# Kernel tuning notes

Measured on AMD Instinct MI355X. Metric: run time of the kernel, lower is better.

The kernel has to match this reference:

```python
import jax, jax.numpy as jnp
import numpy as np

N_NODES = 50000
N_EDGES = 800000
IN_DIM = 128
NUM_GRAPHS = 64
NEG_SLOPE = 0.2  # PyG GATConv default


def _gat_layer(x, src, dst, W, a_s, a_d, b):
    """PyG GATConv (concat=True), eval mode (no dropout).
    x: [N, Fin]; W: [H*C, Fin]; a_s, a_d: [H, C]; b: [H*C]."""
    N = x.shape[0]
    H, C = a_s.shape
    h = (x @ W.T).reshape(N, H, C)                      # [N,H,C]
    es = jnp.einsum('nhc,hc->nh', h, a_s)               # [N,H]
    ed = jnp.einsum('nhc,hc->nh', h, a_d)               # [N,H]
    e = jax.nn.leaky_relu(es[src] + ed[dst], NEG_SLOPE)  # [E,H]
    # segment softmax over incoming edges of each destination node
    m = jax.ops.segment_max(e, dst, num_segments=N)     # [N,H]
    ex = jnp.exp(e - m[dst])
    denom = jax.ops.segment_sum(ex, dst, num_segments=N)
    alpha = ex / denom[dst]                             # [E,H]
    out = jax.ops.segment_sum(h[src] * alpha[:, :, None], dst, num_segments=N)
    return out.reshape(N, H * C) + b


def _make_params(key):
    dims = [(512, IN_DIM, 8, 64), (256, 512, 8, 32), (128, 256, 8, 16), (512, 128, 8, 64)]
    ps = {}
    k = key
    for i, (out_f, in_f, H, C) in enumerate(dims, 1):
        k, k1, k2, k3 = jax.random.split(k, 4)
        s = 1.0 / np.sqrt(in_f)
        ps[f'W{i}'] = jax.random.normal(k1, (out_f, in_f), jnp.float32) * s
        ps[f'a{i}s'] = jax.random.normal(k2, (H, C), jnp.float32) * 0.1
        ps[f'a{i}d'] = jax.random.normal(k3, (H, C), jnp.float32) * 0.1
        ps[f'b{i}'] = jnp.zeros((out_f,), jnp.float32)
    k, k1, k2 = jax.random.split(k, 3)
    ps['lw1'] = jax.random.normal(k1, (32, 512), jnp.float32) * (1.0 / np.sqrt(512))
    ps['lb1'] = jnp.zeros((32,), jnp.float32)
    ps['lw2'] = jax.random.normal(k2, (2, 32), jnp.float32) * (1.0 / np.sqrt(32))
    ps['lb2'] = jnp.zeros((2,), jnp.float32)
    return ps


def setup_inputs() -> dict:
    key = jax.random.key(0)
    kx, ke, kb, kp = jax.random.split(key, 4)
    x = jax.random.normal(kx, (N_NODES, IN_DIM), jnp.float32)
    edge_index = jax.random.randint(ke, (2, N_EDGES), 0, N_NODES, jnp.int64 if jax.config.jax_enable_x64 else jnp.int32)
    batch = jnp.sort(jax.random.randint(kb, (N_NODES,), 0, NUM_GRAPHS, edge_index.dtype))
    inp = {'x': x, 'edge_index': edge_index, 'batch': batch}
    inp.update(_make_params(kp))
    return inp


def reference(x, edge_index, batch,
              W1, a1s, a1d, b1, W2, a2s, a2d, b2,
              W3, a3s, a3d, b3, W4, a4s, a4d, b4,
              lw1, lb1, lw2, lb2):
    N = x.shape[0]
    # PyG GATConv add_self_loops=True
    loop = jnp.arange(N, dtype=edge_index.dtype)
    src = jnp.concatenate([edge_index[0], loop])
    dst = jnp.concatenate([edge_index[1], loop])

    h = jax.nn.elu(_gat_layer(x, src, dst, W1, a1s, a1d, b1))
    h = jax.nn.elu(_gat_layer(h, src, dst, W2, a2s, a2d, b2))
    h = jax.nn.elu(_gat_layer(h, src, dst, W3, a3s, a3d, b3))
    h = _gat_layer(h, src, dst, W4, a4s, a4d, b4)

    # global mean pool over graphs
    sums = jax.ops.segment_sum(h, batch, num_segments=NUM_GRAPHS)
    cnts = jax.ops.segment_sum(jnp.ones((N, 1), h.dtype), batch, num_segments=NUM_GRAPHS)
    g = sums / jnp.maximum(cnts, 1.0)                   # [G, 512]

    g = jax.nn.elu(g @ lw1.T + lb1)                     # dropout skipped (eval)
    return g @ lw2.T + lb2                              # [G, 2]
```

## Files before the change

### kernel.cpp

```cpp
#include <hip/hip_runtime.h>
#include <math.h>

#define NN 50000
#define NE 800000
#define NEP (NE + NN)
#define NGR 64
#define NHEAD 8
#define MPAD 50048

typedef short short8 __attribute__((ext_vector_type(8)));
typedef float floatx4 __attribute__((ext_vector_type(4)));
typedef unsigned uintx4 __attribute__((ext_vector_type(4)));

__device__ inline float bf2f(short s) {
    union { unsigned u; float f; } v;
    v.u = ((unsigned)(unsigned short)s) << 16;
    return v.f;
}
__device__ inline float bf2f_lo(unsigned p) {
    union { unsigned u; float f; } v; v.u = p << 16; return v.f;
}
__device__ inline float bf2f_hi(unsigned p) {
    union { unsigned u; float f; } v; v.u = p & 0xffff0000u; return v.f;
}
__device__ inline short f2bf(float f) {
    union { float f; unsigned u; } v; v.f = f;
    unsigned r = v.u + 0x7fffu + ((v.u >> 16) & 1u);
    return (short)(r >> 16);
}

__global__ void count_deg(const int* __restrict__ ei, int* __restrict__ deg) {
    int e = blockIdx.x * 256 + threadIdx.x;
    if (e >= NEP) return;
    int d = (e < NE) ? ei[NE + e] : (e - NE);
    atomicAdd(&deg[d], 1);
}

__global__ __launch_bounds__(1024) void scan_local(const int* __restrict__ deg,
                                                   int* __restrict__ out,
                                                   int* __restrict__ bsum, int n) {
    __shared__ int sd[1024];
    int b = blockIdx.x, t = threadIdx.x;
    int i = b * 1024 + t;
    int v = (i < n) ? deg[i] : 0;
    sd[t] = v;
    __syncthreads();
    for (int off = 1; off < 1024; off <<= 1) {
        int tmp = (t >= off) ? sd[t - off] : 0;
        __syncthreads();
        sd[t] += tmp;
        __syncthreads();
    }
    if (i < n) out[i] = sd[t] - v;
    if (t == 1023) bsum[b] = sd[1023];
}

__global__ void scan_bsum(int* __restrict__ bsum, int nb) {
    if (threadIdx.x == 0) {
        int s = 0;
        for (int i = 0; i < nb; i++) { int v = bsum[i]; bsum[i] = s; s += v; }
        bsum[nb] = s;
    }
}

__global__ void scan_add(int* __restrict__ row_ptr, int* __restrict__ cursor,
                         const int* __restrict__ bsum, int n, int nb) {
    int i = blockIdx.x * 256 + threadIdx.x;
    if (i < n) {
        int v = row_ptr[i] + bsum[i >> 10];
        row_ptr[i] = v;
        cursor[i] = v;
    } else if (i == n) {
        row_ptr[n] = bsum[nb];
    }
}

__global__ void scatter_edges(const int* __restrict__ ei, int* __restrict__ cursor,
                              int* __restrict__ srcs) {
    int e = blockIdx.x * 256 + threadIdx.x;
    if (e >= NEP) return;
    int s, d;
    if (e < NE) { s = ei[e]; d = ei[NE + e]; }
    else        { s = e - NE; d = e - NE; }
    int pos = atomicAdd(&cursor[d], 1);
    srcs[pos] = s;
}

__global__ void conv_f2bf(const float* __restrict__ in, short* __restrict__ out, int n) {
    int i = blockIdx.x * 256 + threadIdx.x;
    if (i < n) out[i] = f2bf(in[i]);
}

__global__ void conv_x_pad4(const float* __restrict__ x, short* __restrict__ xb) {
    int i = blockIdx.x * 256 + threadIdx.x;
    if (i >= MPAD * 32) return;
    int r = i >> 5;
    short4 o;
    if (r < NN) {
        float4 v = *(const float4*)&x[(size_t)i * 4];
        o.x = f2bf(v.x); o.y = f2bf(v.y); o.z = f2bf(v.z); o.w = f2bf(v.w);
    } else {
        o.x = o.y = o.z = o.w = 0;
    }
    *(short4*)&xb[(size_t)i * 4] = o;
}

#define LDA 72
template <int C>
__global__ __launch_bounds__(256) void gemm_bf(const short* __restrict__ A,
                                               const short* __restrict__ B,
                                               short* __restrict__ Cout,
                                               const float* __restrict__ a_s,
                                               const float* __restrict__ a_d,
                                               float* __restrict__ es,
                                               float* __restrict__ ed,
                                               int K) {
    constexpr int Nc = 8 * C;
    constexpr int colTiles = Nc / 128;
    constexpr int JPH = C / 16;
    constexpr int HPW = 64 / C;
    __shared__ __align__(16) short As[128 * LDA];
    __shared__ __align__(16) short Bs[128 * LDA];
    int bx = blockIdx.x % colTiles;
    int by = blockIdx.x / colTiles;
    int row0 = by * 128, col0 = bx * 128;
    int t = threadIdx.x;
    int lane = t & 63, w = t >> 6;
    int wr = (w >> 1) * 64, wc = (w & 1) * 64;
    int lrow = lane & 15, lq = lane >> 4;

    floatx4 acc[4][4];
#pragma unroll
    for (int i = 0; i < 4; i++)
#pragma unroll
        for (int j = 0; j < 4; j++) acc[i][j] = (floatx4)0.0f;

    for (int k0 = 0; k0 < K; k0 += 64) {
#pragma unroll
        for (int i = 0; i < 4; i++) {
            int chunk = t + i * 256;
            int r = chunk >> 3;
            int kc = (chunk & 7) * 8;
            *(short8*)&As[r * LDA + kc] = *(const short8*)&A[(size_t)(row0 + r) * K + k0 + kc];
            *(short8*)&Bs[r * LDA + kc] = *(const short8*)&B[(size_t)(col0 + r) * K + k0 + kc];
        }
        __syncthreads();
#pragma unroll
        for (int kk = 0; kk < 2; kk++) {
            short8 af[4], bfr[4];
#pragma unroll
            for (int i = 0; i < 4; i++)
                af[i] = *(const short8*)&As[(wr + i * 16 + lrow) * LDA + kk * 32 + lq * 8];
#pragma unroll
            for (int j = 0; j < 4; j++)
                bfr[j] = *(const short8*)&Bs[(wc + j * 16 + lrow) * LDA + kk * 32 + lq * 8];
#pragma unroll
            for (int i = 0; i < 4; i++)
#pragma unroll
                for (int j = 0; j < 4; j++)
                    acc[i][j] = __builtin_amdgcn_mfma_f32_16x16x32_bf16(af[i], bfr[j], acc[i][j], 0, 0, 0);
        }
        __syncthreads();
    }

#pragma unroll
    for (int i = 0; i < 4; i++)
#pragma unroll
        for (int j = 0; j < 4; j++)
#pragma unroll
            for (int r = 0; r < 4; r++) {
                int row = row0 + wr + i * 16 + lq * 4 + r;
                int col = col0 + wc + j * 16 + lrow;
                Cout[(size_t)row * Nc + col] = f2bf(acc[i][j][r]);
            }

    float asv[4], adv[4];
#pragma unroll
    for (int j = 0; j < 4; j++) {
        int colA = col0 + wc + j * 16 + lrow;
        asv[j] = a_s[colA];
        adv[j] = a_d[colA];
    }
    int hb = (col0 + wc) / C;
#pragma unroll
    for (int i = 0; i < 4; i++)
#pragma unroll
        for (int r = 0; r < 4; r++) {
            float s_h[HPW], d_h[HPW];
#pragma unroll
            for (int hh = 0; hh < HPW; hh++) { s_h[hh] = 0.f; d_h[hh] = 0.f; }
#pragma unroll
            for (int j = 0; j < 4; j++) {
                s_h[j / JPH] = fmaf(acc[i][j][r], asv[j], s_h[j / JPH]);
                d_h[j / JPH] = fmaf(acc[i][j][r], adv[j], d_h[j / JPH]);
            }
#pragma unroll
            for (int hh = 0; hh < HPW; hh++) {
#pragma unroll
                for (int off = 1; off <= 8; off <<= 1) {
                    s_h[hh] += __shfl_xor(s_h[hh], off);
                    d_h[hh] += __shfl_xor(d_h[hh], off);
                }
            }
            if (lrow == 0) {
                int row = row0 + wr + i * 16 + lq * 4 + r;
                if (row < NN) {
#pragma unroll
                    for (int hh = 0; hh < HPW; hh++) {
                        es[row * 8 + hb + hh] = s_h[hh];
                        ed[row * 8 + hb + hh] = d_h[hh];
                    }
                }
            }
        }
}

template <int C, bool ELU>
__global__ __launch_bounds__(256) void attn_wave(const short* __restrict__ h,
                                                 const float* __restrict__ es,
                                                 const float* __restrict__ ed,
                                                 const int* __restrict__ row_ptr,
                                                 const int* __restrict__ srcs,
                                                 const float* __restrict__ bias,
                                                 short* __restrict__ out) {
    constexpr int HC = NHEAD * C;
    constexpr int TPR = HC / 8;
    constexpr int EPI = 64 / TPR;
    int wave = threadIdx.x >> 6, lane = threadIdx.x & 63;
    int n = blockIdx.x * 4 + wave;
    int start = row_ptr[n];
    int deg = row_ptr[n + 1] - start;
    int hh1 = lane & 7;
    float edv = ed[n * 8 + hh1];

    float pm = -1e30f;
    for (int idx = lane; idx < deg * 8; idx += 64) {
        int s = srcs[start + (idx >> 3)];
        float e = es[s * 8 + hh1] + edv;
        e = e > 0.f ? e : 0.2f * e;
        pm = fmaxf(pm, e);
    }
    pm = fmaxf(pm, __shfl_xor(pm, 8));
    pm = fmaxf(pm, __shfl_xor(pm, 16));
    pm = fmaxf(pm, __shfl_xor(pm, 32));

    float ps = 0.f;
    for (int idx = lane; idx < deg * 8; idx += 64) {
        int s = srcs[start + (idx >> 3)];
        float e = es[s * 8 + hh1] + edv;
        e = e > 0.f ? e : 0.2f * e;
        ps += __expf(e - pm);
    }
    ps += __shfl_xor(ps, 8);
    ps += __shfl_xor(ps, 16);
    ps += __shfl_xor(ps, 32);
    float invd = 1.0f / ps;

    int sub = lane & (TPR - 1);
    int c0 = sub * 8;
    int hh = c0 / C;
    float mh3 = __shfl(pm, hh);
    float iv3 = __shfl(invd, hh);
    float ed3 = __shfl(edv, hh);

    float acc[8];
#pragma unroll
    for (int j = 0; j < 8; j++) acc[j] = 0.f;

    for (int k = lane / TPR; k < deg; k += EPI) {
        int s = srcs[start + k];
        float e = es[s * 8 + hh] + ed3;
        e = e > 0.f ? e : 0.2f * e;
        float wv = __expf(e - mh3) * iv3;
        uintx4 hv = *(const uintx4*)&h[(size_t)s * HC + c0];
#pragma unroll
        for (int j = 0; j < 4; j++) {
            acc[2 * j]     = fmaf(wv, bf2f_lo(hv[j]), acc[2 * j]);
            acc[2 * j + 1] = fmaf(wv, bf2f_hi(hv[j]), acc[2 * j + 1]);
        }
    }
    if (EPI >= 2) {
#pragma unroll
        for (int j = 0; j < 8; j++) acc[j] += __shfl_xor(acc[j], 32);
    }
    if (EPI == 4) {
#pragma unroll
        for (int j = 0; j < 8; j++) acc[j] += __shfl_xor(acc[j], 16);
    }
    if (lane < TPR) {
        floatx4 b0 = *(const floatx4*)&bias[c0];
        floatx4 b1 = *(const floatx4*)&bias[c0 + 4];
        float bb[8] = {b0[0], b0[1], b0[2], b0[3], b1[0], b1[1], b1[2], b1[3]};
        unsigned pk[4];
#pragma unroll
        for (int j = 0; j < 4; j++) {
            float o0 = acc[2 * j] + bb[2 * j];
            float o1 = acc[2 * j + 1] + bb[2 * j + 1];
            if (ELU) {
                o0 = o0 > 0.f ? o0 : (__expf(o0) - 1.0f);
                o1 = o1 > 0.f ? o1 : (__expf(o1) - 1.0f);
            }
            pk[j] = ((unsigned)(unsigned short)f2bf(o0)) |
                    (((unsigned)(unsigned short)f2bf(o1)) << 16);
        }
        *(uintx4*)&out[(size_t)n * HC + c0] = *(uintx4*)pk;
    }
}

__global__ __launch_bounds__(256) void pool_kernel(const short* __restrict__ h,
                                                   const int* __restrict__ batch,
                                                   float* __restrict__ gout) {
    __shared__ float red[256];
    int g = blockIdx.x >> 3;
    int fc = (blockIdx.x & 7) * 64;
    int lo = 0, hi = NN;
    while (lo < hi) { int mid = (lo + hi) >> 1; if (batch[mid] < g) lo = mid + 1; else hi = mid; }
    int s = lo;
    lo = 0; hi = NN;
    while (lo < hi) { int mid = (lo + hi) >> 1; if (batch[mid] < g + 1) lo = mid + 1; else hi = mid; }
    int e = lo;
    int t = threadIdx.x;
    int f = t & 63, stripe = t >> 6;
    float a = 0.f;
    for (int r = s + stripe; r < e; r += 4)
        a += bf2f(h[(size_t)r * 512 + fc + f]);
    red[t] = a;
    __syncthreads();
    if (t < 128) red[t] += red[t + 128];
    __syncthreads();
    if (t < 64) {
        float inv = 1.0f / fmaxf((float)(e - s), 1.0f);
        gout[g * 512 + fc + t] = (red[t] + red[t + 64]) * inv;
    }
}

__global__ __launch_bounds__(64) void mlp_kernel(const float* __restrict__ g,
                                                 const float* __restrict__ lw1,
                                                 const float* __restrict__ lb1,
                                                 const float* __restrict__ lw2,
                                                 const float* __restrict__ lb2,
                                                 float* __restrict__ outp) {
    __shared__ float gv[512];
    __shared__ float y1[32];
    int b = blockIdx.x, t = threadIdx.x;
    for (int i = t; i < 512; i += 64) gv[i] = g[b * 512 + i];
    __syncthreads();
    if (t < 32) {
        float a = lb1[t];
        for (int k = 0; k < 512; k++) a = fmaf(gv[k], lw1[t * 512 + k], a);
        y1[t] = a > 0.f ? a : (__expf(a) - 1.0f);
    }
    __syncthreads();
    if (t < 2) {
        float a = lb2[t];
        for (int k = 0; k < 32; k++) a = fmaf(y1[k], lw2[t * 32 + k], a);
        outp[b * 2 + t] = a;
    }
}

extern "C" void kernel_launch(void* const* d_in, const int* in_sizes, int n_in,
                              void* d_out, int out_size, void* d_ws, size_t ws_size,
                              hipStream_t stream) {
    (void)in_sizes; (void)n_in; (void)out_size; (void)ws_size;
    const float* x     = (const float*)d_in[0];
    const int*   ei    = (const int*)d_in[1];
    const int*   batch = (const int*)d_in[2];
    const float* W[4]  = {(const float*)d_in[3], (const float*)d_in[7],
                          (const float*)d_in[11], (const float*)d_in[15]};
    const float* As_[4] = {(const float*)d_in[4], (const float*)d_in[8],
                           (const float*)d_in[12], (const float*)d_in[16]};
    const float* Ad_[4] = {(const float*)d_in[5], (const float*)d_in[9],
                           (const float*)d_in[13], (const float*)d_in[17]};
    const float* Bi[4]  = {(const float*)d_in[6], (const float*)d_in[10],
                           (const float*)d_in[14], (const float*)d_in[18]};
    const float* lw1 = (const float*)d_in[19];
    const float* lb1 = (const float*)d_in[20];
    const float* lw2 = (const float*)d_in[21];
    const float* lb2 = (const float*)d_in[22];
    float* out = (float*)d_out;

    short* Ab = (short*)d_ws;
    short* Hb = Ab + (size_t)MPAD * 512;
    short* Wb = Hb + (size_t)MPAD * 512;
    short* Wb_[4] = {Wb, Wb + 65536, Wb + 196608, Wb + 229376};
    const int wsz[4] = {65536, 131072, 32768, 65536};
    float* esb  = (float*)(Wb + 294912);
    float* edb  = esb + NN * NHEAD;
    float* gbuf = edb + NN * NHEAD;
    int* row_ptr = (int*)(gbuf + NGR * 512);
    int* cursor  = row_ptr + (NN + 1);
    int* srcs    = cursor + (NN + 1);
    int* bsum    = srcs + NEP;

    const int nblk = (NN + 1023) / 1024;

    hipMemsetAsync(cursor, 0, NN * sizeof(int), stream);
    count_deg<<<(NEP + 255) / 256, 256, 0, stream>>>(ei, cursor);
    scan_local<<<nblk, 1024, 0, stream>>>(cursor, row_ptr, bsum, NN);
    scan_bsum<<<1, 64, 0, stream>>>(bsum, nblk);
    scan_add<<<(NN + 256) / 256, 256, 0, stream>>>(row_ptr, cursor, bsum, NN, nblk);
    scatter_edges<<<(NEP + 255) / 256, 256, 0, stream>>>(ei, cursor, srcs);

    conv_x_pad4<<<(MPAD * 32 + 255) / 256, 256, 0, stream>>>(x, Ab);
    for (int i = 0; i < 4; i++)
        conv_f2bf<<<(wsz[i] + 255) / 256, 256, 0, stream>>>(W[i], Wb_[i], wsz[i]);

    const int rowTiles = MPAD / 128;
    const int ag = NN / 4;

    gemm_bf<64><<<rowTiles * 4, 256, 0, stream>>>(Ab, Wb_[0], Hb, As_[0], Ad_[0], esb, edb, 128);
    attn_wave<64, true><<<ag, 256, 0, stream>>>(Hb, esb, edb, row_ptr, srcs, Bi[0], Ab);

    gemm_bf<32><<<rowTiles * 2, 256, 0, stream>>>(Ab, Wb_[1], Hb, As_[1], Ad_[1], esb, edb, 512);
    attn_wave<32, true><<<ag, 256, 0, stream>>>(Hb, esb, edb, row_ptr, srcs, Bi[1], Ab);

    gemm_bf<16><<<rowTiles * 1, 256, 0, stream>>>(Ab, Wb_[2], Hb, As_[2], Ad_[2], esb, edb, 256);
    attn_wave<16, true><<<ag, 256, 0, stream>>>(Hb, esb, edb, row_ptr, srcs, Bi[2], Ab);

    gemm_bf<64><<<rowTiles * 4, 256, 0, stream>>>(Ab, Wb_[3], Hb, As_[3], Ad_[3], esb, edb, 128);
    attn_wave<64, false><<<ag, 256, 0, stream>>>(Hb, esb, edb, row_ptr, srcs, Bi[3], Ab);

    pool_kernel<<<NGR * 8, 256, 0, stream>>>(Ab, batch, gbuf);
    mlp_kernel<<<NGR, 64, 0, stream>>>(gbuf, lw1, lb1, lw2, lb2, out);
}
```

Baseline: 878.4 us.

## Use direct global-to-LDS loads with XOR swizzle and online softmax in attention

The GEMM tile loads now use global_load_lds to copy straight from global memory into shared memory, skipping the register round trip. The padded LDS layout is replaced by an XOR-swizzled layout to avoid bank conflicts. The attention kernel merges its max and sum passes into one online-softmax pass with a shuffle-based merge, and the aggregation loop is unrolled by two. The online softmax adds extra exp calls per edge but avoids reading the edge sources and scores a second time.

```diff
diff --git a/kernel.cpp b/kernel.cpp
--- a/kernel.cpp
+++ b/kernel.cpp
@@ -27,6 +27,12 @@
     union { float f; unsigned u; } v; v.f = f;
     unsigned r = v.u + 0x7fffu + ((v.u >> 16) & 1u);
     return (short)(r >> 16);
+}
+
+__device__ inline void gl_lds16(const short* g, short* l) {
+    __builtin_amdgcn_global_load_lds(
+        (const __attribute__((address_space(1))) unsigned int*)g,
+        (__attribute__((address_space(3))) unsigned int*)l, 16, 0, 0);
 }
 
 __global__ void count_deg(const int* __restrict__ ei, int* __restrict__ deg) {
@@ -105,7 +111,6 @@
     *(short4*)&xb[(size_t)i * 4] = o;
 }
 
-#define LDA 72
 template <int C>
 __global__ __launch_bounds__(256) void gemm_bf(const short* __restrict__ A,
                                                const short* __restrict__ B,
@@ -119,8 +124,8 @@
     constexpr int colTiles = Nc / 128;
     constexpr int JPH = C / 16;
     constexpr int HPW = 64 / C;
-    __shared__ __align__(16) short As[128 * LDA];
-    __shared__ __align__(16) short Bs[128 * LDA];
+    __shared__ __align__(16) short As[128 * 64];
+    __shared__ __align__(16) short Bs[128 * 64];
     int bx = blockIdx.x % colTiles;
     int by = blockIdx.x / colTiles;
     int row0 = by * 128, col0 = bx * 128;
@@ -129,6 +134,9 @@
     int wr = (w >> 1) * 64, wc = (w & 1) * 64;
     int lrow = lane & 15, lq = lane >> 4;
 
+    int srow = lane >> 3;
+    int kcsrc = (lane & 7) ^ srow;
+
     floatx4 acc[4][4];
 #pragma unroll
     for (int i = 0; i < 4; i++)
@@ -137,23 +145,23 @@
 
     for (int k0 = 0; k0 < K; k0 += 64) {
 #pragma unroll
-        for (int i = 0; i < 4; i++) {
-            int chunk = t + i * 256;
-            int r = chunk >> 3;
-            int kc = (chunk & 7) * 8;
-            *(short8*)&As[r * LDA + kc] = *(const short8*)&A[(size_t)(row0 + r) * K + k0 + kc];
-            *(short8*)&Bs[r * LDA + kc] = *(const short8*)&B[(size_t)(col0 + r) * K + k0 + kc];
+        for (int it = 0; it < 4; it++) {
+            int r0 = w * 32 + it * 8;
+            int r = r0 + srow;
+            gl_lds16(&A[(size_t)(row0 + r) * K + k0 + kcsrc * 8], &As[r0 * 64]);
+            gl_lds16(&B[(size_t)(col0 + r) * K + k0 + kcsrc * 8], &Bs[r0 * 64]);
         }
         __syncthreads();
 #pragma unroll
         for (int kk = 0; kk < 2; kk++) {
+            int slot = (kk * 4 + lq) ^ (lrow & 7);
             short8 af[4], bfr[4];
 #pragma unroll
             for (int i = 0; i < 4; i++)
-                af[i] = *(const short8*)&As[(wr + i * 16 + lrow) * LDA + kk * 32 + lq * 8];
+                af[i] = *(const short8*)&As[(wr + i * 16 + lrow) * 64 + slot * 8];
 #pragma unroll
             for (int j = 0; j < 4; j++)
-                bfr[j] = *(const short8*)&Bs[(wc + j * 16 + lrow) * LDA + kk * 32 + lq * 8];
+                bfr[j] = *(const short8*)&Bs[(wc + j * 16 + lrow) * 64 + slot * 8];
 #pragma unroll
             for (int i = 0; i < 4; i++)
 #pragma unroll
@@ -233,27 +241,23 @@
     int hh1 = lane & 7;
     float edv = ed[n * 8 + hh1];
 
-    float pm = -1e30f;
+    float pm = -1e30f, ps = 0.f;
     for (int idx = lane; idx < deg * 8; idx += 64) {
         int s = srcs[start + (idx >> 3)];
         float e = es[s * 8 + hh1] + edv;
         e = e > 0.f ? e : 0.2f * e;
-        pm = fmaxf(pm, e);
-    }
-    pm = fmaxf(pm, __shfl_xor(pm, 8));
-    pm = fmaxf(pm, __shfl_xor(pm, 16));
-    pm = fmaxf(pm, __shfl_xor(pm, 32));
-
-    float ps = 0.f;
-    for (int idx = lane; idx < deg * 8; idx += 64) {
-        int s = srcs[start + (idx >> 3)];
-        float e = es[s * 8 + hh1] + edv;
-        e = e > 0.f ? e : 0.2f * e;
-        ps += __expf(e - pm);
-    }
-    ps += __shfl_xor(ps, 8);
-    ps += __shfl_xor(ps, 16);
-    ps += __shfl_xor(ps, 32);
+        float mn = fmaxf(pm, e);
+        ps = ps * __expf(pm - mn) + __expf(e - mn);
+        pm = mn;
+    }
+#pragma unroll
+    for (int off = 8; off <= 32; off <<= 1) {
+        float mo = __shfl_xor(pm, off);
+        float so = __shfl_xor(ps, off);
+        float mn = fmaxf(pm, mo);
+        ps = ps * __expf(pm - mn) + so * __expf(mo - mn);
+        pm = mn;
+    }
     float invd = 1.0f / ps;
 
     int sub = lane & (TPR - 1);
@@ -267,6 +271,7 @@
 #pragma unroll
     for (int j = 0; j < 8; j++) acc[j] = 0.f;
 
+#pragma unroll 2
     for (int k = lane / TPR; k < deg; k += EPI) {
         int s = srcs[start + k];
         float e = es[s * 8 + hh] + ed3;
```

Result: faster. 813.2 us (-7.4%).
